# Performance work log

Hardware: AMD Instinct MI355X
Metric: run time of the kernel (lower is better)

## Reference

```python
import jax, jax.numpy as jnp
import numpy as np

D_MODEL = 1024
NUM_SLOTS = 64
TOP_K = 8
B, T = 4, 4096


def setup_inputs() -> dict:
    key = jax.random.key(0)
    ks = jax.random.split(key, 16)
    D, S = D_MODEL, NUM_SLOTS
    H = D // 2  # route MLP hidden (hardcoded d_model//2 in source)
    sc = lambda fan_in: 1.0 / np.sqrt(fan_in)
    inp = {
        "x": jax.random.normal(ks[0], (B, T, D), dtype=jnp.float32),
        # learned params
        "slot_init": jax.random.normal(ks[1], (S, D), dtype=jnp.float32) * 0.1,
        "slot_scale": jnp.ones((S, 1), dtype=jnp.float32),
        "w1": jax.random.normal(ks[2], (H, 2 * D), dtype=jnp.float32) * sc(2 * D),
        "b1": jnp.zeros((H,), dtype=jnp.float32),
        "w2": jax.random.normal(ks[3], (S, H), dtype=jnp.float32) * sc(H),
        "b2": jnp.zeros((S,), dtype=jnp.float32),
        "gru_wih": jax.random.normal(ks[4], (3 * D, D), dtype=jnp.float32) * sc(D),
        "gru_whh": jax.random.normal(ks[5], (3 * D, D), dtype=jnp.float32) * sc(D),
        "gru_bih": jnp.zeros((3 * D,), dtype=jnp.float32),
        "gru_bhh": jnp.zeros((3 * D,), dtype=jnp.float32),
        "wv": jax.random.normal(ks[6], (D, D), dtype=jnp.float32) * sc(D),
        "bv": jnp.zeros((D,), dtype=jnp.float32),
        "wo": jax.random.normal(ks[7], (D, D), dtype=jnp.float32) * sc(D),
        "bo": jnp.zeros((D,), dtype=jnp.float32),
        "tau": jnp.ones((1,), dtype=jnp.float32),
    }
    return inp


def _forward(x, slot_init, slot_scale, w1, b1, w2, b2,
             gru_wih, gru_whh, gru_bih, gru_bhh, wv, bv, wo, bo, tau):
    Bn, Tn, D = x.shape
    Sn = slot_init.shape[0]
    # initial slot states, expanded over batch: (B, S, D)
    S = jnp.broadcast_to((slot_init * slot_scale)[None], (Bn, Sn, D)).astype(x.dtype)
    slot_mean = S.mean(axis=1, keepdims=True)                      # (B,1,D)
    ctx = jnp.concatenate([x, jnp.broadcast_to(slot_mean, x.shape)], axis=-1)  # (B,T,2D)
    h = jax.nn.gelu(ctx @ w1.T + b1, approximate=False)
    route_logits = (h @ w2.T + b2) / (jnp.abs(tau) + 0.1)          # (B,T,S)
    topk_vals, topk_idx = jax.lax.top_k(route_logits, TOP_K)
    topk_w = jax.nn.softmax(topk_vals, axis=-1)                    # (B,T,K)
    # scatter top-k weights into dense alpha (B,T,S)
    alpha = jnp.sum(topk_w[..., None] * jax.nn.one_hot(topk_idx, Sn, dtype=x.dtype), axis=-2)
    slot_input = jnp.einsum('bts,btd->bsd', alpha, x)              # dispatch
    slot_wsum = alpha.sum(axis=1) + 1e-8                           # (B,S)
    gi = (slot_input / slot_wsum[..., None]).reshape(Bn * Sn, D)
    hs = S.reshape(Bn * Sn, D)
    # GRUCell (torch semantics)
    gx = gi @ gru_wih.T + gru_bih                                  # (BS, 3D)
    gh = hs @ gru_whh.T + gru_bhh
    xr, xz, xn = jnp.split(gx, 3, axis=-1)
    hr, hz, hn = jnp.split(gh, 3, axis=-1)
    r = jax.nn.sigmoid(xr + hr)
    z = jax.nn.sigmoid(xz + hz)
    n = jnp.tanh(xn + r * hn)
    h_new = (1.0 - z) * n + z * hs
    S_new = h_new.reshape(Bn, Sn, D)
    slot_values = S_new @ wv.T + bv                                # (B,S,D)
    out = jnp.einsum('bts,bsd->btd', alpha, slot_values)           # combine
    return out @ wo.T + bo


def reference(x, slot_init, slot_scale, w1, b1, w2, b2,
              gru_wih, gru_whh, gru_bih, gru_bhh, wv, bv, wo, bo, tau):
    return _forward(x, slot_init, slot_scale, w1, b1, w2, b2,
                    gru_wih, gru_whh, gru_bih, gru_bhh, wv, bv, wo, bo, tau)
```

## Files before the change

kernel.cpp:

```cpp
#include <hip/hip_runtime.h>

using u16 = unsigned short;
using u32 = unsigned int;

typedef __attribute__((ext_vector_type(8))) short bf16x8;
typedef __attribute__((ext_vector_type(4))) float f32x4;

#define NTOK 16384

constexpr size_t OFF_FLAG   = 0;
constexpr size_t OFF_FCNT   = 256;
constexpr size_t OFF_M      = 512;
constexpr size_t OFF_B1P64  = 8704;
constexpr size_t OFF_B1P32  = 12800;
constexpr size_t OFF_B2F    = 14848;
constexpr size_t OFF_BIHF   = 15104;
constexpr size_t OFF_BHHF   = 27392;
constexpr size_t OFF_BVF    = 39680;
constexpr size_t OFF_BOF    = 43776;
constexpr size_t OFF_FLAGS  = 47872;
constexpr size_t OFF_HSHI   = 113408;
constexpr size_t OFF_HSLO   = 244480;
constexpr size_t OFF_HSF    = 375552;
constexpr size_t OFF_GH     = 637696;
constexpr size_t OFF_GIHI   = 1424128;
constexpr size_t OFF_GILO   = 1948416;
constexpr size_t OFF_GX     = 2472704;
constexpr size_t OFF_SNHI   = 5618432;
constexpr size_t OFF_SNLO   = 6142720;
constexpr size_t OFF_SVHI   = 6667008;
constexpr size_t OFF_SVLO   = 7191296;
constexpr size_t OFF_SVO    = 7715584;
constexpr size_t OFF_IDX    = 8764160;
constexpr size_t OFF_WGT    = 9288448;
constexpr size_t OFF_LOGITS = 9812736;
constexpr size_t OFF_W1HI   = 14007040;
constexpr size_t OFF_W1LO   = 16104192;
constexpr size_t OFF_W2HI   = 18201344;
constexpr size_t OFF_W2LO   = 18266880;
constexpr size_t OFF_WIHHI  = 18332416;
constexpr size_t OFF_WIHLO  = 24623872;
constexpr size_t OFF_WHHHI  = 30915328;
constexpr size_t OFF_WHHLO  = 37206784;
constexpr size_t OFF_WVHI   = 43498240;
constexpr size_t OFF_WVLO   = 45595392;
constexpr size_t OFF_WOHI   = 47692544;
constexpr size_t OFF_WOLO   = 49789696;
constexpr size_t OFF_HHI    = 51886848;
constexpr size_t OFF_HLO    = 68664064;
constexpr size_t OFF_DPART  = 85441280;
constexpr size_t OFF_DWSUM  = 93829888;
constexpr size_t OFF_HSMG   = 93838080;
constexpr size_t WS_NEED    = 94886656;

constexpr int QCAP = 256;

__device__ __forceinline__ float bf2f(u16 u) {
  union { u32 i; float f; } c; c.i = ((u32)u) << 16; return c.f;
}
__device__ __forceinline__ u16 f2bf(float f) {
  u32 x = __float_as_uint(f);
  x += 0x7fffu + ((x >> 16) & 1u);
  return (u16)(x >> 16);
}
__device__ __forceinline__ void splitf(float v, u16& hi, u16& lo) {
  hi = f2bf(v);
  lo = f2bf(v - bf2f(hi));
}
__device__ __forceinline__ float rdval(const void* p, int i, int f32m) {
  return f32m ? ((const float*)p)[i] : bf2f(((const u16*)p)[i]);
}
__device__ __forceinline__ void async16(const u16* g, u16* l) {
  __builtin_amdgcn_global_load_lds((const __attribute__((address_space(1))) void*)g,
                                   (__attribute__((address_space(3))) void*)l, 16, 0, 0);
}

__global__ void k_sniff(const u32* __restrict__ w1w, int* __restrict__ flag) {
  int t = threadIdx.x;
  u32 word = w1w[t * 97];
  int ef = (word >> 7) & 0xFF;
  unsigned long long m = __ballot(ef >= 128);
  if (t == 0) flag[0] = (__popcll(m) >= 8) ? 1 : 0;
}

__global__ __launch_bounds__(256) void k_cvt_all(
    const void* __restrict__ w1, const void* __restrict__ w2,
    const void* __restrict__ wih, const void* __restrict__ whh,
    const void* __restrict__ wv, const void* __restrict__ wo,
    const void* __restrict__ b2, const void* __restrict__ bih,
    const void* __restrict__ bhh, const void* __restrict__ bv,
    const void* __restrict__ bo, char* __restrict__ ws,
    const int* __restrict__ flagp)
{
  const int f = *flagp;
  const long long gid = (long long)blockIdx.x * 256 + threadIdx.x;
  const long long C0 = 1048576, C1 = C0 + 32768, C2 = C1 + 3145728,
                  C3 = C2 + 3145728, C4 = C3 + 1048576, C5 = C4 + 1048576;
  if (gid < C5) {
    const void* src; size_t oh, ol; int i;
    if (gid < C0)      { src = w1;  oh = OFF_W1HI;  ol = OFF_W1LO;  i = (int)gid; }
    else if (gid < C1) { src = w2;  oh = OFF_W2HI;  ol = OFF_W2LO;  i = (int)(gid - C0); }
    else if (gid < C2) { src = wih; oh = OFF_WIHHI; ol = OFF_WIHLO; i = (int)(gid - C1); }
    else if (gid < C3) { src = whh; oh = OFF_WHHHI; ol = OFF_WHHLO; i = (int)(gid - C2); }
    else if (gid < C4) { src = wv;  oh = OFF_WVHI;  ol = OFF_WVLO;  i = (int)(gid - C3); }
    else               { src = wo;  oh = OFF_WOHI;  ol = OFF_WOLO;  i = (int)(gid - C4); }
    float v = rdval(src, i, f);
    u16 hi, lo; splitf(v, hi, lo);
    ((u16*)(ws + oh))[i] = hi;
    ((u16*)(ws + ol))[i] = lo;
    return;
  }
  int r = (int)(gid - C5);
  if (r >= 8256) return;
  const void* src; size_t od; int i;
  if (r < 64)        { src = b2;  od = OFF_B2F;  i = r; }
  else if (r < 3136) { src = bih; od = OFF_BIHF; i = r - 64; }
  else if (r < 6208) { src = bhh; od = OFF_BHHF; i = r - 3136; }
  else if (r < 7232) { src = bv;  od = OFF_BVF;  i = r - 6208; }
  else               { src = bo;  od = OFF_BOF;  i = r - 7232; }
  ((float*)(ws + od))[i] = rdval(src, i, f);
}

template<int MODE>
__global__ __launch_bounds__(512, 2) void gemm_bt(
    const u16* __restrict__ Ahi, const u16* __restrict__ Alo,
    const u16* __restrict__ Bhi, const u16* __restrict__ Blo,
    int M, int N, int K, int ldb,
    const float* __restrict__ biasF, float* __restrict__ outF,
    u16* __restrict__ outHi, u16* __restrict__ outLo)
{
  __shared__ alignas(16) u16 smem[2 * 2 * 8192];
  const int t    = threadIdx.x;
  const int grp  = t >> 8;
  const int tl   = t & 255;
  const int wvid = tl >> 6;
  const int lane = t & 63;
  const int quad = lane >> 4;
  const int l16  = lane & 15;
  const int row0 = blockIdx.x * 128;
  const int col0 = blockIdx.y * 128;
  const int wr   = (wvid >> 1) * 64;
  const int wc   = (wvid & 1) * 64;

  const int ra  = tl >> 2;
  const int kqe = (tl & 3) * 8;
  int r_a0 = row0 + ra;      if (r_a0 > M - 1) r_a0 = M - 1;
  int r_a1 = row0 + ra + 64; if (r_a1 > M - 1) r_a1 = M - 1;
  int r_b0 = col0 + ra;      if (r_b0 > N - 1) r_b0 = N - 1;
  int r_b1 = col0 + ra + 64; if (r_b1 > N - 1) r_b1 = N - 1;
  const size_t aoff0 = (size_t)r_a0 * K + kqe;
  const size_t aoff1 = (size_t)r_a1 * K + kqe;
  const size_t boff0 = (size_t)r_b0 * ldb + kqe;
  const size_t boff1 = (size_t)r_b1 * ldb + kqe;

  const int KH  = K >> 1;
  const int NIT = 3 * (KH >> 5);
  int sp = 0, sk = grp * KH;
  const int skend = grp * KH + KH;

  u16* const base = smem + grp * 16384;
  auto stage = [&](int buf) {
    const u16* Ap = (sp == 1) ? Alo : Ahi;
    const u16* Bp = (sp == 2) ? Blo : Bhi;
    u16* At = base + buf * 8192;
    u16* Bt = At + 4096;
    async16(Ap + aoff0 + sk, &At[(wvid * 64) * 8]);
    async16(Ap + aoff1 + sk, &At[(wvid * 64 + 256) * 8]);
    async16(Bp + boff0 + sk, &Bt[(wvid * 64) * 8]);
    async16(Bp + boff1 + sk, &Bt[(wvid * 64 + 256) * 8]);
    sk += 32;
    if (sk == skend) { sk = grp * KH; ++sp; }
  };

  f32x4 acc[4][4] = {};
  stage(0);
  asm volatile("s_waitcnt vmcnt(0)" ::: "memory");
  __syncthreads();
  int cur = 0;
  for (int it = 0; it < NIT; ++it) {
    if (it + 1 < NIT) stage(cur ^ 1);
    const u16* At = base + cur * 8192;
    const u16* Bt = At + 4096;
    bf16x8 af[4], bfr[4];
    #pragma unroll
    for (int mt = 0; mt < 4; ++mt)
      af[mt] = *(const bf16x8*)&At[(wr + mt * 16 + l16) * 32 + quad * 8];
    #pragma unroll
    for (int nt = 0; nt < 4; ++nt)
      bfr[nt] = *(const bf16x8*)&Bt[(wc + nt * 16 + l16) * 32 + quad * 8];
    #pragma unroll
    for (int mt = 0; mt < 4; ++mt)
      #pragma unroll
      for (int nt = 0; nt < 4; ++nt)
        acc[mt][nt] = __builtin_amdgcn_mfma_f32_16x16x32_bf16(
            af[mt], bfr[nt], acc[mt][nt], 0, 0, 0);
    asm volatile("s_waitcnt vmcnt(0)" ::: "memory");
    __syncthreads();
    cur ^= 1;
  }

  float* red = (float*)smem;
  #pragma unroll 1
  for (int half = 0; half < 2; ++half) {
    if (grp == 1 && (wvid & 1) == half) {
      #pragma unroll
      for (int mt = 0; mt < 4; ++mt)
        #pragma unroll
        for (int nt = 0; nt < 4; ++nt)
          #pragma unroll
          for (int r2 = 0; r2 < 4; ++r2)
            red[(wr + mt * 16 + quad * 4 + r2) * 64 + nt * 16 + l16] =
                acc[mt][nt][r2];
    }
    __syncthreads();
    if (grp == 0 && (wvid & 1) == half) {
      #pragma unroll
      for (int mt = 0; mt < 4; ++mt)
        #pragma unroll
        for (int nt = 0; nt < 4; ++nt)
          #pragma unroll
          for (int r2 = 0; r2 < 4; ++r2)
            acc[mt][nt][r2] +=
                red[(wr + mt * 16 + quad * 4 + r2) * 64 + nt * 16 + l16];
    }
    __syncthreads();
  }
  if (grp != 0) return;

  #pragma unroll
  for (int mt = 0; mt < 4; ++mt) {
    #pragma unroll
    for (int nt = 0; nt < 4; ++nt) {
      const int col = col0 + wc + nt * 16 + l16;
      if (col >= N) continue;
      #pragma unroll
      for (int r2 = 0; r2 < 4; ++r2) {
        const int row = row0 + wr + mt * 16 + quad * 4 + r2;
        if (row >= M) continue;
        float v = acc[mt][nt][r2] + biasF[col];
        size_t idx = (size_t)row * N + col;
        if constexpr (MODE == 0) {
          outF[idx] = v;
        } else {
          u16 hi, lo; splitf(v, hi, lo);
          outHi[idx] = hi; outLo[idx] = lo;
        }
      }
    }
  }
}

__global__ __launch_bounds__(256, 4) void gemm_router(
    const void* __restrict__ X,
    const u16* __restrict__ Bhi, const u16* __restrict__ Blo,
    int M, int N, int K, int ldb, const float* __restrict__ biasF,
    u16* __restrict__ outHi, u16* __restrict__ outLo,
    const int* __restrict__ flagp)
{
  __shared__ alignas(16) u16 Athi[64 * 32];
  __shared__ alignas(16) u16 Atlo[64 * 32];
  __shared__ alignas(16) u16 Bthi[128 * 32];
  __shared__ alignas(16) u16 Btlo[128 * 32];
  const int f32m = *flagp;
  const int t    = threadIdx.x;
  const int wvid = t >> 6;
  const int lane = t & 63;
  const int quad = lane >> 4;
  const int l16  = lane & 15;
  const int row0 = blockIdx.x * 64;
  const int col0 = blockIdx.y * 128;
  const int wr   = (wvid >> 1) * 32;
  const int wc   = (wvid & 1) * 64;

  const int ra  = t >> 2;
  const int kqe = (t & 3) * 8;
  int r_b0 = col0 + ra;      if (r_b0 > N - 1) r_b0 = N - 1;
  int r_b1 = col0 + ra + 64; if (r_b1 > N - 1) r_b1 = N - 1;
  const u16* gBhi0 = Bhi + (size_t)r_b0 * ldb + kqe;
  const u16* gBhi1 = Bhi + (size_t)r_b1 * ldb + kqe;
  const u16* gBlo0 = Blo + (size_t)r_b0 * ldb + kqe;
  const u16* gBlo1 = Blo + (size_t)r_b1 * ldb + kqe;
  const float* Xf = (const float*)X;
  const u16*   Xb = (const u16*)X;

  f32x4 acc[2][4] = {};

  for (int k0 = 0; k0 < K; k0 += 32) {
    async16(gBhi0 + k0, &Bthi[(wvid * 64) * 8]);
    async16(gBhi1 + k0, &Bthi[(wvid * 64 + 256) * 8]);
    async16(gBlo0 + k0, &Btlo[(wvid * 64) * 8]);
    async16(gBlo1 + k0, &Btlo[(wvid * 64 + 256) * 8]);
    #pragma unroll
    for (int i = 0; i < 2; ++i) {
      int j = t + 256 * i;
      int row = j >> 3, kq = (j & 7) * 4;
      int grow = row0 + row; if (grow > M - 1) grow = M - 1;
      ushort4 hi4, lo4;
      if (f32m) {
        const float4 v = *(const float4*)(Xf + (size_t)grow * K + k0 + kq);
        splitf(v.x, hi4.x, lo4.x);
        splitf(v.y, hi4.y, lo4.y);
        splitf(v.z, hi4.z, lo4.z);
        splitf(v.w, hi4.w, lo4.w);
      } else {
        hi4 = *(const ushort4*)(Xb + (size_t)grow * K + k0 + kq);
        lo4.x = lo4.y = lo4.z = lo4.w = 0;
      }
      *(ushort4*)&Athi[row * 32 + kq] = hi4;
      *(ushort4*)&Atlo[row * 32 + kq] = lo4;
    }
    asm volatile("s_waitcnt vmcnt(0)" ::: "memory");
    __syncthreads();
    bf16x8 ah[2], al[2], bh[4], bl[4];
    #pragma unroll
    for (int mt = 0; mt < 2; ++mt) {
      ah[mt] = *(const bf16x8*)&Athi[(wr + mt * 16 + l16) * 32 + quad * 8];
      al[mt] = *(const bf16x8*)&Atlo[(wr + mt * 16 + l16) * 32 + quad * 8];
    }
    #pragma unroll
    for (int nt = 0; nt < 4; ++nt) {
      bh[nt] = *(const bf16x8*)&Bthi[(wc + nt * 16 + l16) * 32 + quad * 8];
      bl[nt] = *(const bf16x8*)&Btlo[(wc + nt * 16 + l16) * 32 + quad * 8];
    }
    #pragma unroll
    for (int mt = 0; mt < 2; ++mt)
      #pragma unroll
      for (int nt = 0; nt < 4; ++nt) {
        acc[mt][nt] = __builtin_amdgcn_mfma_f32_16x16x32_bf16(
            ah[mt], bh[nt], acc[mt][nt], 0, 0, 0);
        acc[mt][nt] = __builtin_amdgcn_mfma_f32_16x16x32_bf16(
            al[mt], bh[nt], acc[mt][nt], 0, 0, 0);
        acc[mt][nt] = __builtin_amdgcn_mfma_f32_16x16x32_bf16(
            ah[mt], bl[nt], acc[mt][nt], 0, 0, 0);
      }
    __syncthreads();
  }

  #pragma unroll
  for (int mt = 0; mt < 2; ++mt) {
    #pragma unroll
    for (int nt = 0; nt < 4; ++nt) {
      const int col = col0 + wc + nt * 16 + l16;
      if (col >= N) continue;
      #pragma unroll
      for (int r2 = 0; r2 < 4; ++r2) {
        const int row = row0 + wr + mt * 16 + quad * 4 + r2;
        if (row >= M) continue;
        float v = acc[mt][nt][r2] + biasF[col];
        v = 0.5f * v * (1.0f + erff(v * 0.70710678118654752f));
        u16 hi, lo; splitf(v, hi, lo);
        size_t idx = (size_t)row * N + col;
        outHi[idx] = hi; outLo[idx] = lo;
      }
    }
  }
}

__global__ __launch_bounds__(256) void k_init(const void* __restrict__ sli,
    const void* __restrict__ slsc, const int* __restrict__ flagp,
    double* __restrict__ m64, int* __restrict__ fcnt,
    u16* __restrict__ hshi, u16* __restrict__ hslo, float* __restrict__ hsf)
{
  int f = *flagp;
  int gid = blockIdx.x * 256 + threadIdx.x;
  if (gid == 0) fcnt[0] = 0;
  if (gid < 1024) {
    double s = 0.0;
    for (int j = 0; j < 64; ++j)
      s += (double)rdval(sli, j * 1024 + gid, f) * (double)rdval(slsc, j, f);
    m64[gid] = s * (1.0 / 64.0);
  }
  for (int i = gid; i < 64 * 1024; i += 16384) {
    int s = i >> 10;
    float v = rdval(sli, i, f) * rdval(slsc, s, f);
    splitf(v, hshi[i], hslo[i]);
    hsf[i] = v;
  }
}

__global__ __launch_bounds__(256) void k_b1p(const void* __restrict__ w1,
    const void* __restrict__ b1, const int* __restrict__ flagp,
    const double* __restrict__ m64, double* __restrict__ b1p64,
    float* __restrict__ b1p32)
{
  int f = *flagp;
  int h = blockIdx.x * 256 + threadIdx.x;
  if (h >= 512) return;
  double a = (double)rdval(b1, h, f);
  if (f) {
    const float* wr = (const float*)w1 + (size_t)h * 2048 + 1024;
    for (int d = 0; d < 1024; ++d) a += (double)wr[d] * m64[d];
  } else {
    const u16* wr = (const u16*)w1 + (size_t)h * 2048 + 1024;
    for (int d = 0; d < 1024; ++d) a += (double)bf2f(wr[d]) * m64[d];
  }
  b1p64[h] = a;
  b1p32[h] = (float)a;
}

__global__ __launch_bounds__(256) void k_topk(const float* __restrict__ logits,
    const void* __restrict__ tau, const int* __restrict__ flagp,
    int* __restrict__ idxb, float* __restrict__ wgtb,
    int* __restrict__ fcnt, int* __restrict__ flags)
{
  const int f32m = *flagp;
  const int n    = blockIdx.x * 4 + (threadIdx.x >> 6);
  const int lane = threadIdx.x & 63;
  float cur = logits[(size_t)n * 64 + lane];
  float tv[8]; int ti[8]; float v9 = 0.f;
  #pragma unroll
  for (int it = 0; it < 9; ++it) {
    float v = cur; int i = lane;
    #pragma unroll
    for (int off = 32; off; off >>= 1) {
      float ov = __shfl_xor(v, off);
      int   oi = __shfl_xor(i, off);
      if (ov > v || (ov == v && oi < i)) { v = ov; i = oi; }
    }
    if (it < 8) { tv[it] = v; ti[it] = i; if (lane == i) cur = -__builtin_inff(); }
    else v9 = v;
  }
  float itau = 1.0f / (fabsf(rdval(tau, 0, f32m)) + 0.1f);
  float e[8], z = 0.f;
  #pragma unroll
  for (int k = 0; k < 8; ++k) { e[k] = expf((tv[k] - tv[0]) * itau); z += e[k]; }
  if (lane == 0) {
    float theta = f32m ? 2e-4f : 1e-4f;
    if (tv[7] - v9 < theta) { int p = atomicAdd(fcnt, 1); flags[p] = n; }
    float rz = 1.0f / z;
    #pragma unroll
    for (int k = 0; k < 8; ++k) {
      idxb[n * 8 + k] = ti[k];
      wgtb[n * 8 + k] = e[k] * rz;
    }
  }
}

__global__ __launch_bounds__(256) void k_repair_h(const void* __restrict__ x,
    const void* __restrict__ w1, const int* __restrict__ flagp,
    const double* __restrict__ b1p64, const int* __restrict__ fcnt,
    const int* __restrict__ flags, double* __restrict__ hsmg)
{
  const int f = *flagp;
  int cnt = *fcnt; if (cnt > QCAP) cnt = QCAP;
  const int q = blockIdx.x >> 3;
  if (q >= cnt) return;
  const int chunk = blockIdx.x & 7;
  const int n  = flags[q];
  const int wv = threadIdx.x >> 6;
  const int lane = threadIdx.x & 63;

  float xr[16];
  if (f) {
    const float* xp = (const float*)x + (size_t)n * 1024;
    #pragma unroll
    for (int j = 0; j < 16; ++j) xr[j] = xp[lane + 64 * j];
  } else {
    const u16* xp = (const u16*)x + (size_t)n * 1024;
    #pragma unroll
    for (int j = 0; j < 16; ++j) xr[j] = bf2f(xp[lane + 64 * j]);
  }

  const int h0 = chunk * 64 + wv * 16;
  for (int r = 0; r < 16; ++r) {
    const int h = h0 + r;
    double a0 = 0.0, a1 = 0.0;
    if (f) {
      const float* wr = (const float*)w1 + (size_t)h * 2048;
      #pragma unroll
      for (int j = 0; j < 16; j += 2) {
        a0 += (double)xr[j]     * (double)wr[lane + 64 * j];
        a1 += (double)xr[j + 1] * (double)wr[lane + 64 * (j + 1)];
      }
    } else {
      const u16* wr = (const u16*)w1 + (size_t)h * 2048;
      #pragma unroll
      for (int j = 0; j < 16; j += 2) {
        a0 += (double)xr[j]     * (double)bf2f(wr[lane + 64 * j]);
        a1 += (double)xr[j + 1] * (double)bf2f(wr[lane + 64 * (j + 1)]);
      }
    }
    double a = a0 + a1;
    #pragma unroll
    for (int off = 32; off; off >>= 1) a += __shfl_xor(a, off);
    if (lane == 0) {
      a += b1p64[h];
      hsmg[(size_t)q * 512 + h] =
          0.5 * a * (1.0 + erf(a * 0.70710678118654752440));
    }
  }
}

__global__ __launch_bounds__(256) void k_repair_t(const void* __restrict__ x,
    const void* __restrict__ w1, const void* __restrict__ w2,
    const void* __restrict__ b2, const void* __restrict__ tau,
    const int* __restrict__ flagp, const double* __restrict__ b1p64,
    const int* __restrict__ fcnt, const int* __restrict__ flags,
    const double* __restrict__ hsmg, int* __restrict__ idxb,
    float* __restrict__ wgtb)
{
  __shared__ double hsm[512];
  __shared__ double lg[64];
  const int f = *flagp;
  const int cnt = *fcnt;
  const int t = threadIdx.x;
  const int wv = t >> 6;
  const int lane = t & 63;
  for (int q = blockIdx.x; q < cnt; q += gridDim.x) {
    const int n = flags[q];
    if (q < QCAP) {
      for (int h = t; h < 512; h += 256) hsm[h] = hsmg[(size_t)q * 512 + h];
    } else {
      for (int h = wv; h < 512; h += 4) {
        double a0 = 0.0, a1 = 0.0;
        if (f) {
          const float* xp = (const float*)x + (size_t)n * 1024;
          const float* wr = (const float*)w1 + (size_t)h * 2048;
          for (int j = 0; j < 16; j += 2) {
            a0 += (double)xp[lane + 64 * j]       * (double)wr[lane + 64 * j];
            a1 += (double)xp[lane + 64 * (j + 1)] * (double)wr[lane + 64 * (j + 1)];
          }
        } else {
          const u16* xp = (const u16*)x + (size_t)n * 1024;
          const u16* wr = (const u16*)w1 + (size_t)h * 2048;
          for (int j = 0; j < 16; j += 2) {
            a0 += (double)bf2f(xp[lane + 64 * j]) * (double)bf2f(wr[lane + 64 * j]);
            a1 += (double)bf2f(xp[lane + 64 * (j + 1)]) *
                  (double)bf2f(wr[lane + 64 * (j + 1)]);
          }
        }
        double a = a0 + a1;
        #pragma unroll
        for (int off = 32; off; off >>= 1) a += __shfl_xor(a, off);
        if (lane == 0) {
          a += b1p64[h];
          hsm[h] = 0.5 * a * (1.0 + erf(a * 0.70710678118654752440));
        }
      }
    }
    __syncthreads();
    for (int s = wv; s < 64; s += 4) {
      double a0 = 0.0, a1 = 0.0;
      if (f) {
        const float* wr = (const float*)w2 + (size_t)s * 512;
        #pragma unroll
        for (int j = 0; j < 8; j += 2) {
          a0 += hsm[lane + 64 * j]       * (double)wr[lane + 64 * j];
          a1 += hsm[lane + 64 * (j + 1)] * (double)wr[lane + 64 * (j + 1)];
        }
      } else {
        const u16* wr = (const u16*)w2 + (size_t)s * 512;
        #pragma unroll
        for (int j = 0; j < 8; j += 2) {
          a0 += hsm[lane + 64 * j]       * (double)bf2f(wr[lane + 64 * j]);
          a1 += hsm[lane + 64 * (j + 1)] * (double)bf2f(wr[lane + 64 * (j + 1)]);
        }
      }
      double a = a0 + a1;
      #pragma unroll
      for (int off = 32; off; off >>= 1) a += __shfl_xor(a, off);
      if (lane == 0) lg[s] = a + (double)rdval(b2, s, f);
    }
    __syncthreads();
    if (t == 0) {
      double tv = fabs((double)rdval(tau, 0, f)) + 0.1;
      double vals[8]; int ids[8];
      for (int it = 0; it < 8; ++it) {
        double best = -1e300; int bi = 0;
        for (int i = 0; i < 64; ++i)
          if (lg[i] > best) { best = lg[i]; bi = i; }
        vals[it] = best; ids[it] = bi; lg[bi] = -1e300;
      }
      double e[8], z = 0.0;
      for (int k = 0; k < 8; ++k) { e[k] = exp((vals[k] - vals[0]) / tv); z += e[k]; }
      for (int k = 0; k < 8; ++k) {
        idxb[n * 8 + k] = ids[k];
        wgtb[n * 8 + k] = (float)(e[k] / z);
      }
    }
    __syncthreads();
  }
}

__global__ __launch_bounds__(256) void k_dispatch(const void* __restrict__ X,
    const int* __restrict__ flagp, const int* __restrict__ idxb,
    const float* __restrict__ wgtb,
    float* __restrict__ dpart, float* __restrict__ dwsum)
{
  __shared__ int   ltok[512];
  __shared__ float lw[512];
  __shared__ int   lcnt;
  __shared__ float lws;
  const int f32m = *flagp;
  const int g    = blockIdx.x;
  const int xcd  = g & 7;
  const int ord  = g >> 3;
  const int win  = xcd * 4 + (ord >> 6);
  const int s    = ord & 63;
  const int b     = win >> 3;
  const int chunk = win & 7;
  const int t     = threadIdx.x;
  if (t == 0) { lcnt = 0; lws = 0.f; }
  __syncthreads();
  const int tok0 = b * 4096 + chunk * 512;
  float mysum = 0.f;
  for (int tok = tok0 + t; tok < tok0 + 512; tok += 256) {
    int hit = -1;
    #pragma unroll
    for (int k = 0; k < 8; ++k)
      if (idxb[(size_t)tok * 8 + k] == s) hit = k;
    if (hit >= 0) {
      float w = wgtb[(size_t)tok * 8 + hit];
      int p = atomicAdd(&lcnt, 1);
      ltok[p] = tok; lw[p] = w;
      mysum += w;
    }
  }
  atomicAdd(&lws, mysum);
  __syncthreads();
  const int cnt = lcnt;
  float a0 = 0.f, a1 = 0.f, a2 = 0.f, a3 = 0.f;
  if (f32m) {
    const float* Xf = (const float*)X;
    for (int e = 0; e < cnt; ++e) {
      int tok = ltok[e]; float w = lw[e];
      const float4 v = *(const float4*)(Xf + (size_t)tok * 1024 + 4 * t);
      a0 += w * v.x; a1 += w * v.y; a2 += w * v.z; a3 += w * v.w;
    }
  } else {
    const u16* Xb = (const u16*)X;
    for (int e = 0; e < cnt; ++e) {
      int tok = ltok[e]; float w = lw[e];
      const ushort4 v = *(const ushort4*)(Xb + (size_t)tok * 1024 + 4 * t);
      a0 += w * bf2f(v.x); a1 += w * bf2f(v.y);
      a2 += w * bf2f(v.z); a3 += w * bf2f(v.w);
    }
  }
  const int bs = b * 64 + s;
  float* pp = dpart + ((size_t)bs * 8 + chunk) * 1024 + 4 * t;
  float4 outv = { a0, a1, a2, a3 };
  *(float4*)pp = outv;
  if (t == 0) dwsum[bs * 8 + chunk] = lws;
}

__global__ __launch_bounds__(256) void k_dreduce(const float* __restrict__ dpart,
    const float* __restrict__ dwsum, u16* __restrict__ gihi, u16* __restrict__ gilo)
{
  const int bs = blockIdx.x;
  const int t  = threadIdx.x;
  float ws = 0.f;
  #pragma unroll
  for (int c = 0; c < 8; ++c) ws += dwsum[bs * 8 + c];
  const float inv = 1.0f / (ws + 1e-8f);
  float a0 = 0.f, a1 = 0.f, a2 = 0.f, a3 = 0.f;
  const float* pb = dpart + (size_t)bs * 8 * 1024 + 4 * t;
  #pragma unroll
  for (int c = 0; c < 8; ++c) {
    const float4 v = *(const float4*)(pb + c * 1024);
    a0 += v.x; a1 += v.y; a2 += v.z; a3 += v.w;
  }
  const size_t base = (size_t)bs * 1024 + 4 * t;
  splitf(a0 * inv, gihi[base + 0], gilo[base + 0]);
  splitf(a1 * inv, gihi[base + 1], gilo[base + 1]);
  splitf(a2 * inv, gihi[base + 2], gilo[base + 2]);
  splitf(a3 * inv, gihi[base + 3], gilo[base + 3]);
}

__global__ __launch_bounds__(256) void k_gru(const float* __restrict__ gx,
    const float* __restrict__ gh, const float* __restrict__ hsf,
    u16* __restrict__ snhi, u16* __restrict__ snlo)
{
  int gid = blockIdx.x * 256 + threadIdx.x;
  int r = gid >> 10, d = gid & 1023, s = r & 63;
  const float* gxr = gx + (size_t)r * 3072;
  const float* ghr = gh + (size_t)s * 3072;
  float rr = 1.0f / (1.0f + expf(-(gxr[d] + ghr[d])));
  float zz = 1.0f / (1.0f + expf(-(gxr[1024 + d] + ghr[1024 + d])));
  float nn = tanhf(gxr[2048 + d] + rr * ghr[2048 + d]);
  float hs = hsf[s * 1024 + d];
  float hv = (1.0f - zz) * nn + zz * hs;
  splitf(hv, snhi[gid], snlo[gid]);
}

__global__ __launch_bounds__(256) void k_out(const int* __restrict__ idxb,
    const float* __restrict__ wgtb, const float* __restrict__ svo,
    const int* __restrict__ flagp, void* __restrict__ out)
{
  const int f32m = *flagp;
  int n = blockIdx.x * 4 + (threadIdx.x >> 6);
  int lane = threadIdx.x & 63;
  int b = n >> 12;
  const float* svb = svo + (size_t)b * 64 * 1024;
  int id[8]; float w[8];
  #pragma unroll
  for (int k = 0; k < 8; ++k) { id[k] = idxb[n * 8 + k]; w[k] = wgtb[n * 8 + k]; }
  #pragma unroll
  for (int i = 0; i < 16; ++i) {
    int d = i * 64 + lane;
    float a = 0.f;
    #pragma unroll
    for (int k = 0; k < 8; ++k) a += w[k] * svb[(size_t)id[k] * 1024 + d];
    size_t idx = (size_t)n * 1024 + d;
    if (f32m) ((float*)out)[idx] = a;
    else      ((u16*)out)[idx] = f2bf(a);
  }
}

extern "C" void kernel_launch(void* const* d_in, const int* in_sizes, int n_in,
                              void* d_out, int out_size, void* d_ws, size_t ws_size,
                              hipStream_t stream) {
  if (ws_size < WS_NEED) {
    hipMemsetAsync(d_out, 0, (size_t)out_size * 2, stream);
    return;
  }
  const void* x    = d_in[0];
  const void* sli  = d_in[1];
  const void* slsc = d_in[2];
  const void* w1   = d_in[3];
  const void* b1   = d_in[4];
  const void* w2   = d_in[5];
  const void* b2   = d_in[6];
  const void* wih  = d_in[7];
  const void* whh  = d_in[8];
  const void* bih  = d_in[9];
  const void* bhh  = d_in[10];
  const void* wv   = d_in[11];
  const void* bv   = d_in[12];
  const void* wo   = d_in[13];
  const void* bo   = d_in[14];
  const void* tau  = d_in[15];
  char* ws = (char*)d_ws;

  int*    flag   = (int*)(ws + OFF_FLAG);
  int*    fcnt   = (int*)(ws + OFF_FCNT);
  double* m64    = (double*)(ws + OFF_M);
  double* b1p64  = (double*)(ws + OFF_B1P64);
  float*  b1p32  = (float*)(ws + OFF_B1P32);
  float*  b2f    = (float*)(ws + OFF_B2F);
  float*  bihf   = (float*)(ws + OFF_BIHF);
  float*  bhhf   = (float*)(ws + OFF_BHHF);
  float*  bvf    = (float*)(ws + OFF_BVF);
  float*  bof    = (float*)(ws + OFF_BOF);
  int*    flags  = (int*)(ws + OFF_FLAGS);
  u16*    hshi   = (u16*)(ws + OFF_HSHI);
  u16*    hslo   = (u16*)(ws + OFF_HSLO);
  float*  hsf    = (float*)(ws + OFF_HSF);
  float*  gh     = (float*)(ws + OFF_GH);
  u16*    gihi   = (u16*)(ws + OFF_GIHI);
  u16*    gilo   = (u16*)(ws + OFF_GILO);
  float*  gx     = (float*)(ws + OFF_GX);
  u16*    snhi   = (u16*)(ws + OFF_SNHI);
  u16*    snlo   = (u16*)(ws + OFF_SNLO);
  u16*    svhi   = (u16*)(ws + OFF_SVHI);
  u16*    svlo   = (u16*)(ws + OFF_SVLO);
  float*  svo    = (float*)(ws + OFF_SVO);
  int*    idxb   = (int*)(ws + OFF_IDX);
  float*  wgtb   = (float*)(ws + OFF_WGT);
  float*  logits = (float*)(ws + OFF_LOGITS);
  u16*    w1hi   = (u16*)(ws + OFF_W1HI);
  u16*    w1lo   = (u16*)(ws + OFF_W1LO);
  u16*    w2hi   = (u16*)(ws + OFF_W2HI);
  u16*    w2lo   = (u16*)(ws + OFF_W2LO);
  u16*    wihhi  = (u16*)(ws + OFF_WIHHI);
  u16*    wihlo  = (u16*)(ws + OFF_WIHLO);
  u16*    whhhi  = (u16*)(ws + OFF_WHHHI);
  u16*    whhlo  = (u16*)(ws + OFF_WHHLO);
  u16*    wvhi   = (u16*)(ws + OFF_WVHI);
  u16*    wvlo   = (u16*)(ws + OFF_WVLO);
  u16*    wohi   = (u16*)(ws + OFF_WOHI);
  u16*    wolo   = (u16*)(ws + OFF_WOLO);
  u16*    hhi    = (u16*)(ws + OFF_HHI);
  u16*    hlo    = (u16*)(ws + OFF_HLO);
  float*  dpart  = (float*)(ws + OFF_DPART);
  float*  dwsum  = (float*)(ws + OFF_DWSUM);
  double* hsmg   = (double*)(ws + OFF_HSMG);

  k_sniff<<<1, 64, 0, stream>>>((const u32*)w1, flag);

  k_init<<<64, 256, 0, stream>>>(sli, slsc, flag, m64, fcnt, hshi, hslo, hsf);
  k_b1p<<<2, 256, 0, stream>>>(w1, b1, flag, m64, b1p64, b1p32);

  k_cvt_all<<<37025, 256, 0, stream>>>(w1, w2, wih, whh, wv, wo,
                                       b2, bih, bhh, bv, bo, ws, flag);

  gemm_bt<0><<<dim3(1, 24), 512, 0, stream>>>(
      hshi, hslo, whhhi, whhlo, 64, 3072, 1024, 1024, bhhf, gh, nullptr, nullptr);

  gemm_router<<<dim3(256, 4), 256, 0, stream>>>(
      x, w1hi, w1lo, NTOK, 512, 1024, 2048, b1p32, hhi, hlo, flag);

  gemm_bt<0><<<dim3(128, 1), 512, 0, stream>>>(
      hhi, hlo, w2hi, w2lo, NTOK, 64, 512, 512, b2f, logits, nullptr, nullptr);

  k_topk<<<4096, 256, 0, stream>>>(logits, tau, flag, idxb, wgtb, fcnt, flags);
  k_repair_h<<<2048, 256, 0, stream>>>(x, w1, flag, b1p64, fcnt, flags, hsmg);
  k_repair_t<<<256, 256, 0, stream>>>(x, w1, w2, b2, tau, flag, b1p64, fcnt,
                                      flags, hsmg, idxb, wgtb);
  k_dispatch<<<2048, 256, 0, stream>>>(x, flag, idxb, wgtb, dpart, dwsum);
  k_dreduce<<<256, 256, 0, stream>>>(dpart, dwsum, gihi, gilo);

  gemm_bt<0><<<dim3(2, 24), 512, 0, stream>>>(
      gihi, gilo, wihhi, wihlo, 256, 3072, 1024, 1024, bihf, gx, nullptr, nullptr);

  k_gru<<<1024, 256, 0, stream>>>(gx, gh, hsf, snhi, snlo);

  gemm_bt<3><<<dim3(2, 8), 512, 0, stream>>>(
      snhi, snlo, wvhi, wvlo, 256, 1024, 1024, 1024, bvf, nullptr, svhi, svlo);

  gemm_bt<0><<<dim3(2, 8), 512, 0, stream>>>(
      svhi, svlo, wohi, wolo, 256, 1024, 1024, 1024, bof, svo, nullptr, nullptr);

  k_out<<<4096, 256, 0, stream>>>(idxb, wgtb, svo, flag, d_out);

  (void)in_sizes; (void)n_in; (void)out_size; (void)ws_size;
}
```

Baseline: 664.0 us.

## Swizzle LDS tiles and double-buffer router B loads

Applies an XOR swizzle to the k-quad offset of the LDS tiles in both the generic bt GEMM and the router GEMM, so fragment reads from rows sharing a bank pattern spread across banks. The router GEMM also double-buffers its B tiles, issuing the async loads for the next k-step before computing the current one, and waits with a partial vmcnt instead of a full drain. This targets LDS bank conflicts and exposed global-load latency, at the cost of more LDS use and hand-tuned waitcnt and barrier logic that could break if the load count or ordering changes.

```diff
diff --git a/kernel.cpp b/kernel.cpp
--- a/kernel.cpp
+++ b/kernel.cpp
@@ -137,13 +137,14 @@
   const int lane = t & 63;
   const int quad = lane >> 4;
   const int l16  = lane & 15;
+  const int qs8  = (quad ^ ((l16 >> 1) & 3)) * 8;
   const int row0 = blockIdx.x * 128;
   const int col0 = blockIdx.y * 128;
   const int wr   = (wvid >> 1) * 64;
   const int wc   = (wvid & 1) * 64;
 
   const int ra  = tl >> 2;
-  const int kqe = (tl & 3) * 8;
+  const int kqe = ((tl & 3) ^ ((ra >> 1) & 3)) * 8;
   int r_a0 = row0 + ra;      if (r_a0 > M - 1) r_a0 = M - 1;
   int r_a1 = row0 + ra + 64; if (r_a1 > M - 1) r_a1 = M - 1;
   int r_b0 = col0 + ra;      if (r_b0 > N - 1) r_b0 = N - 1;
@@ -184,10 +185,10 @@
     bf16x8 af[4], bfr[4];
     #pragma unroll
     for (int mt = 0; mt < 4; ++mt)
-      af[mt] = *(const bf16x8*)&At[(wr + mt * 16 + l16) * 32 + quad * 8];
+      af[mt] = *(const bf16x8*)&At[(wr + mt * 16 + l16) * 32 + qs8];
     #pragma unroll
     for (int nt = 0; nt < 4; ++nt)
-      bfr[nt] = *(const bf16x8*)&Bt[(wc + nt * 16 + l16) * 32 + quad * 8];
+      bfr[nt] = *(const bf16x8*)&Bt[(wc + nt * 16 + l16) * 32 + qs8];
     #pragma unroll
     for (int mt = 0; mt < 4; ++mt)
       #pragma unroll
@@ -259,21 +260,22 @@
 {
   __shared__ alignas(16) u16 Athi[64 * 32];
   __shared__ alignas(16) u16 Atlo[64 * 32];
-  __shared__ alignas(16) u16 Bthi[128 * 32];
-  __shared__ alignas(16) u16 Btlo[128 * 32];
+  __shared__ alignas(16) u16 Bthi[2][128 * 32];
+  __shared__ alignas(16) u16 Btlo[2][128 * 32];
   const int f32m = *flagp;
   const int t    = threadIdx.x;
   const int wvid = t >> 6;
   const int lane = t & 63;
   const int quad = lane >> 4;
   const int l16  = lane & 15;
+  const int qs8  = (quad ^ ((l16 >> 1) & 3)) * 8;
   const int row0 = blockIdx.x * 64;
   const int col0 = blockIdx.y * 128;
   const int wr   = (wvid >> 1) * 32;
   const int wc   = (wvid & 1) * 64;
 
   const int ra  = t >> 2;
-  const int kqe = (t & 3) * 8;
+  const int kqe = ((t & 3) ^ ((ra >> 1) & 3)) * 8;
   int r_b0 = col0 + ra;      if (r_b0 > N - 1) r_b0 = N - 1;
   int r_b1 = col0 + ra + 64; if (r_b1 > N - 1) r_b1 = N - 1;
   const u16* gBhi0 = Bhi + (size_t)r_b0 * ldb + kqe;
@@ -285,15 +287,18 @@
 
   f32x4 acc[2][4] = {};
 
+  async16(gBhi0, &Bthi[0][(wvid * 64) * 8]);
+  async16(gBhi1, &Bthi[0][(wvid * 64 + 256) * 8]);
+  async16(gBlo0, &Btlo[0][(wvid * 64) * 8]);
+  async16(gBlo1, &Btlo[0][(wvid * 64 + 256) * 8]);
+
+  int cur = 0;
   for (int k0 = 0; k0 < K; k0 += 32) {
-    async16(gBhi0 + k0, &Bthi[(wvid * 64) * 8]);
-    async16(gBhi1 + k0, &Bthi[(wvid * 64 + 256) * 8]);
-    async16(gBlo0 + k0, &Btlo[(wvid * 64) * 8]);
-    async16(gBlo1 + k0, &Btlo[(wvid * 64 + 256) * 8]);
     #pragma unroll
     for (int i = 0; i < 2; ++i) {
       int j = t + 256 * i;
       int row = j >> 3, kq = (j & 7) * 4;
+      int swidx = row * 32 + (kq & 7) + ((((kq >> 3) ^ ((row >> 1) & 3))) << 3);
       int grow = row0 + row; if (grow > M - 1) grow = M - 1;
       ushort4 hi4, lo4;
       if (f32m) {
@@ -306,21 +311,29 @@
         hi4 = *(const ushort4*)(Xb + (size_t)grow * K + k0 + kq);
         lo4.x = lo4.y = lo4.z = lo4.w = 0;
       }
-      *(ushort4*)&Athi[row * 32 + kq] = hi4;
-      *(ushort4*)&Atlo[row * 32 + kq] = lo4;
-    }
-    asm volatile("s_waitcnt vmcnt(0)" ::: "memory");
-    __syncthreads();
+      *(ushort4*)&Athi[swidx] = hi4;
+      *(ushort4*)&Atlo[swidx] = lo4;
+    }
+    __builtin_amdgcn_sched_barrier(0);
+    if (k0 + 32 < K) {
+      const int nb = cur ^ 1;
+      async16(gBhi0 + k0 + 32, &Bthi[nb][(wvid * 64) * 8]);
+      async16(gBhi1 + k0 + 32, &Bthi[nb][(wvid * 64 + 256) * 8]);
+      async16(gBlo0 + k0 + 32, &Btlo[nb][(wvid * 64) * 8]);
+      async16(gBlo1 + k0 + 32, &Btlo[nb][(wvid * 64 + 256) * 8]);
+    }
+    asm volatile("s_waitcnt vmcnt(4) lgkmcnt(0)" ::: "memory");
+    __builtin_amdgcn_s_barrier();
     bf16x8 ah[2], al[2], bh[4], bl[4];
     #pragma unroll
     for (int mt = 0; mt < 2; ++mt) {
-      ah[mt] = *(const bf16x8*)&Athi[(wr + mt * 16 + l16) * 32 + quad * 8];
-      al[mt] = *(const bf16x8*)&Atlo[(wr + mt * 16 + l16) * 32 + quad * 8];
+      ah[mt] = *(const bf16x8*)&Athi[(wr + mt * 16 + l16) * 32 + qs8];
+      al[mt] = *(const bf16x8*)&Atlo[(wr + mt * 16 + l16) * 32 + qs8];
     }
     #pragma unroll
     for (int nt = 0; nt < 4; ++nt) {
-      bh[nt] = *(const bf16x8*)&Bthi[(wc + nt * 16 + l16) * 32 + quad * 8];
-      bl[nt] = *(const bf16x8*)&Btlo[(wc + nt * 16 + l16) * 32 + quad * 8];
+      bh[nt] = *(const bf16x8*)&Bthi[cur][(wc + nt * 16 + l16) * 32 + qs8];
+      bl[nt] = *(const bf16x8*)&Btlo[cur][(wc + nt * 16 + l16) * 32 + qs8];
     }
     #pragma unroll
     for (int mt = 0; mt < 2; ++mt)
@@ -333,7 +346,8 @@
         acc[mt][nt] = __builtin_amdgcn_mfma_f32_16x16x32_bf16(
             ah[mt], bl[nt], acc[mt][nt], 0, 0, 0);
       }
-    __syncthreads();
+    __builtin_amdgcn_s_barrier();
+    cur ^= 1;
   }
 
   #pragma unroll
```

New measurement: 713.4 us. 1.07x slower.
